# Kernel optimization log

Hardware: AMD Instinct MI355X
Metric: run time of the kernel (lower is better)

Reference implementation:

```python
import jax, jax.numpy as jnp
import numpy as np

N, E, F_IN, HID, HEADS, OUT, NGRAPH = 50000, 800000, 128, 64, 4, 64, 512
NEG_SLOPE = 0.2


def setup_inputs() -> dict:
    key = jax.random.key(0)
    ks = jax.random.split(key, 16)
    d1 = HID * HEADS  # 256
    inp = {
        "x": jax.random.normal(ks[0], (N, F_IN), jnp.float32),
        "edge_index": jax.random.randint(ks[1], (2, E), 0, N, jnp.int64),
        "batch": jnp.sort(jax.random.randint(ks[2], (N,), 0, NGRAPH, jnp.int64)),
        # layer 1 params (GATConv(F_IN -> HID, heads=HEADS, concat=True))
        "W1": jax.random.normal(ks[3], (F_IN, d1), jnp.float32) * 0.05,
        "att_src1": jax.random.normal(ks[4], (HEADS, HID), jnp.float32) * 0.05,
        "att_dst1": jax.random.normal(ks[5], (HEADS, HID), jnp.float32) * 0.05,
        "b1": jnp.zeros((d1,), jnp.float32),
        # layer 2 params (GATConv(d1 -> HID, heads=HEADS, concat=True))
        "W2": jax.random.normal(ks[6], (d1, d1), jnp.float32) * 0.05,
        "att_src2": jax.random.normal(ks[7], (HEADS, HID), jnp.float32) * 0.05,
        "att_dst2": jax.random.normal(ks[8], (HEADS, HID), jnp.float32) * 0.05,
        "b2": jnp.zeros((d1,), jnp.float32),
        # final linear
        "fc_w": jax.random.normal(ks[9], (d1, OUT), jnp.float32) * 0.05,
        "fc_b": jnp.zeros((OUT,), jnp.float32),
    }
    return inp


def _gat_layer(x, src, dst, W, att_src, att_dst, bias):
    # linear transform, split into heads: [N, H, C]
    h = (x @ W).reshape(N, HEADS, HID)
    # per-node attention logits (a^T h), per head: [N, H]
    a_s = jnp.einsum("nhc,hc->nh", h, att_src)
    a_d = jnp.einsum("nhc,hc->nh", h, att_dst)
    # per-edge logits with leaky relu: [E', H]
    e = a_s[src] + a_d[dst]
    e = jnp.where(e > 0, e, NEG_SLOPE * e)
    # segment softmax over edges grouped by destination node
    m = jax.ops.segment_max(e, dst, num_segments=N)
    ex = jnp.exp(e - m[dst])
    s = jax.ops.segment_sum(ex, dst, num_segments=N)
    alpha = ex / s[dst]  # every node has a self-loop -> s > 0
    # weighted message aggregation: scatter-add of alpha * h_src
    out = jax.ops.segment_sum(h[src] * alpha[:, :, None], dst, num_segments=N)
    return out.reshape(N, HEADS * HID) + bias


def reference(x, edge_index, batch, W1, att_src1, att_dst1, b1,
              W2, att_src2, att_dst2, b2, fc_w, fc_b):
    # PyG GATConv default add_self_loops=True
    loop = jnp.arange(N, dtype=edge_index.dtype)
    src = jnp.concatenate([edge_index[0], loop])
    dst = jnp.concatenate([edge_index[1], loop])

    h = _gat_layer(x, src, dst, W1, att_src1, att_dst1, b1)
    h = jax.nn.elu(h)  # dropout is identity in eval mode
    h = _gat_layer(h, src, dst, W2, att_src2, att_dst2, b2)
    h = jax.nn.elu(h)

    # global mean pool over graphs
    sums = jax.ops.segment_sum(h, batch, num_segments=NGRAPH)
    cnts = jax.ops.segment_sum(jnp.ones((N,), h.dtype), batch, num_segments=NGRAPH)
    pooled = sums / jnp.maximum(cnts, 1.0)[:, None]

    return pooled @ fc_w + fc_b
```

## Files before the change

### kernel.cpp

```cpp
#include <hip/hip_runtime.h>
#include <cstddef>
#include <cstdint>

#define NN 50000
#define EE 800000
#define ETOT (EE + NN)
#define FIN 128
#define D1 256
#define HID 64
#define HEADS 4
#define NG 512
#define FOUT 64
#define NEG_SLOPE 0.2f

typedef _Float16 f16x8 __attribute__((ext_vector_type(8)));
typedef _Float16 f16x4 __attribute__((ext_vector_type(4)));
typedef float f32x4 __attribute__((ext_vector_type(4)));

__device__ __forceinline__ float leaky(float x) { return x > 0.f ? x : NEG_SLOPE * x; }

__global__ void k_hist(const int* __restrict__ ei, int* __restrict__ deg) {
    int e = blockIdx.x * 256 + threadIdx.x;
    if (e < EE) atomicAdd(&deg[ei[EE + e]], 1);
}

__global__ void k_scan_blocks(const int* __restrict__ deg, int* __restrict__ row_off,
                              int* __restrict__ part) {
    __shared__ int sd[256];
    int tid = threadIdx.x;
    int i = blockIdx.x * 256 + tid;
    int v = (i < NN) ? deg[i] + 1 : 0;
    sd[tid] = v;
    __syncthreads();
    for (int off = 1; off < 256; off <<= 1) {
        int t = (tid >= off) ? sd[tid - off] : 0;
        __syncthreads();
        sd[tid] += t;
        __syncthreads();
    }
    if (i < NN) row_off[i] = sd[tid] - v;
    if (tid == 255) part[blockIdx.x] = sd[255];
}

__global__ void k_scan_part(int* __restrict__ part) {
    __shared__ int sd[256];
    int tid = threadIdx.x;
    int nblk = (NN + 255) / 256;
    int v = (tid < nblk) ? part[tid] : 0;
    sd[tid] = v;
    __syncthreads();
    for (int off = 1; off < 256; off <<= 1) {
        int t = (tid >= off) ? sd[tid - off] : 0;
        __syncthreads();
        sd[tid] += t;
        __syncthreads();
    }
    part[tid] = sd[tid] - v;
}

__global__ void k_add_off(int* __restrict__ row_off, const int* __restrict__ part,
                          int* __restrict__ cursor) {
    int i = blockIdx.x * 256 + threadIdx.x;
    if (i < NN) {
        int r = row_off[i] + part[blockIdx.x];
        row_off[i] = r;
        cursor[i] = r;
    }
    if (i == 0) row_off[NN] = ETOT;
}

__global__ void k_scatter(const int* __restrict__ ei, int* __restrict__ cursor,
                          int* __restrict__ csr_src) {
    int i = blockIdx.x * 256 + threadIdx.x;
    if (i < ETOT) {
        int s, d;
        if (i < EE) { s = ei[i]; d = ei[EE + i]; }
        else        { s = d = i - EE; }
        int p = atomicAdd(&cursor[d], 1);
        csr_src[p] = s;
    }
}

__global__ void k_cvt_w(const float* __restrict__ W1, const float* __restrict__ W2,
                        _Float16* __restrict__ w1t, _Float16* __restrict__ w2t) {
    int idx = blockIdx.x * 256 + threadIdx.x;
    if (idx < 256 * FIN) {
        int n = idx / FIN, k = idx - n * FIN;
        w1t[idx] = (_Float16)W1[(size_t)k * 256 + n];
    } else if (idx < 256 * FIN + 256 * D1) {
        int j = idx - 256 * FIN;
        int n = j >> 8, k = j & 255;
        w2t[j] = (_Float16)W2[(size_t)k * 256 + n];
    }
}

#define BM 128
#define BN 128
#define BK 64
#define LDK (BK + 4)

template <int K, typename AT>
__global__ __launch_bounds__(256) void k_gemm(const AT* __restrict__ A,
                                              const _Float16* __restrict__ Bt,
                                              _Float16* __restrict__ C,
                                              const float* __restrict__ att_s,
                                              const float* __restrict__ att_d,
                                              float* __restrict__ a_s,
                                              float* __restrict__ a_d) {
    __shared__ _Float16 As[BM][LDK];
    __shared__ _Float16 Bs[BN][LDK];
    const int tid = threadIdx.x;
    const int lane = tid & 63;
    const int wave = tid >> 6;
    const int wm = wave & 1, wn = wave >> 1;
    const int m0 = blockIdx.x * BM;
    const int n0 = blockIdx.y * BN;
    const int row_m = lane & 15, quad = lane >> 4;

    f32x4 acc[4][4];
#pragma unroll
    for (int mi = 0; mi < 4; ++mi)
#pragma unroll
        for (int ni = 0; ni < 4; ++ni)
#pragma unroll
            for (int r = 0; r < 4; ++r) acc[mi][ni][r] = 0.f;

    const int c8 = (tid & 7) * 8;
    const int rr = tid >> 3;

    for (int k0 = 0; k0 < K; k0 += BK) {
#pragma unroll
        for (int p = 0; p < 4; ++p) {
            int r = p * 32 + rr;
            int gr = m0 + r; gr = gr < NN ? gr : NN - 1;
            f16x8 o;
            if constexpr (sizeof(AT) == 4) {
                const float4 v0 = *(const float4*)((const float*)A + (size_t)gr * K + k0 + c8);
                const float4 v1 = *(const float4*)((const float*)A + (size_t)gr * K + k0 + c8 + 4);
                o[0] = (_Float16)v0.x; o[1] = (_Float16)v0.y;
                o[2] = (_Float16)v0.z; o[3] = (_Float16)v0.w;
                o[4] = (_Float16)v1.x; o[5] = (_Float16)v1.y;
                o[6] = (_Float16)v1.z; o[7] = (_Float16)v1.w;
            } else {
                o = *(const f16x8*)((const _Float16*)A + (size_t)gr * K + k0 + c8);
            }
            *(f16x8*)(&As[r][c8]) = o;
        }
#pragma unroll
        for (int p = 0; p < 4; ++p) {
            int r = p * 32 + rr;
            f16x8 v = *(const f16x8*)(Bt + (size_t)(n0 + r) * K + k0 + c8);
            *(f16x8*)(&Bs[r][c8]) = v;
        }
        __syncthreads();
#pragma unroll
        for (int kc = 0; kc < BK; kc += 32) {
            f16x8 af[4], bf[4];
#pragma unroll
            for (int mi = 0; mi < 4; ++mi)
                af[mi] = *(const f16x8*)(&As[wm * 64 + mi * 16 + row_m][kc + quad * 8]);
#pragma unroll
            for (int ni = 0; ni < 4; ++ni)
                bf[ni] = *(const f16x8*)(&Bs[wn * 64 + ni * 16 + row_m][kc + quad * 8]);
#pragma unroll
            for (int mi = 0; mi < 4; ++mi)
#pragma unroll
                for (int ni = 0; ni < 4; ++ni)
                    acc[mi][ni] = __builtin_amdgcn_mfma_f32_16x16x32_f16(
                        bf[ni], af[mi], acc[mi][ni], 0, 0, 0);
        }
        __syncthreads();
    }
#pragma unroll
    for (int mi = 0; mi < 4; ++mi) {
        int m = m0 + wm * 64 + mi * 16 + row_m;
        if (m < NN) {
#pragma unroll
            for (int ni = 0; ni < 4; ++ni) {
                f16x4 o;
                o[0] = (_Float16)acc[mi][ni][0];
                o[1] = (_Float16)acc[mi][ni][1];
                o[2] = (_Float16)acc[mi][ni][2];
                o[3] = (_Float16)acc[mi][ni][3];
                *(f16x4*)(C + (size_t)m * D1 + n0 + wn * 64 + ni * 16 + quad * 4) = o;
            }
        }
    }
    const int head = blockIdx.y * 2 + wn;
    const float* attsv = att_s + head * HID;
    const float* attdv = att_d + head * HID;
    float avs[4][4], avd[4][4];
#pragma unroll
    for (int ni = 0; ni < 4; ++ni)
#pragma unroll
        for (int r = 0; r < 4; ++r) {
            avs[ni][r] = attsv[ni * 16 + quad * 4 + r];
            avd[ni][r] = attdv[ni * 16 + quad * 4 + r];
        }
#pragma unroll
    for (int mi = 0; mi < 4; ++mi) {
        float ps = 0.f, pd = 0.f;
#pragma unroll
        for (int ni = 0; ni < 4; ++ni)
#pragma unroll
            for (int r = 0; r < 4; ++r) {
                ps += acc[mi][ni][r] * avs[ni][r];
                pd += acc[mi][ni][r] * avd[ni][r];
            }
        ps += __shfl_xor(ps, 16); ps += __shfl_xor(ps, 32);
        pd += __shfl_xor(pd, 16); pd += __shfl_xor(pd, 32);
        int m = m0 + wm * 64 + mi * 16 + row_m;
        if (quad == 0 && m < NN) {
            a_s[m * 4 + head] = ps;
            a_d[m * 4 + head] = pd;
        }
    }
}

__global__ __launch_bounds__(64) void k_aggregate(
    const _Float16* __restrict__ h, const float* __restrict__ a_s,
    const float* __restrict__ a_d, const int* __restrict__ row_off,
    const int* __restrict__ csr_src, const float* __restrict__ bias,
    _Float16* __restrict__ out, int apply_elu) {
    const int n = blockIdx.x;
    const int tid = threadIdx.x;
    const int myhead = tid >> 4;
    const int start = row_off[n];
    const int end = row_off[n + 1];

    __shared__ float s_w[64][4];
    __shared__ int s_src[64];

    const float4 ad = *(const float4*)(a_d + (size_t)n * 4);

    float l0 = 0.f, l1 = 0.f, l2 = 0.f, l3 = 0.f;
    float4 acc = make_float4(0.f, 0.f, 0.f, 0.f);
    const int c4 = tid * 4;
    for (int base = start; base < end; base += 64) {
        int len = min(64, end - base);
        if (tid < len) {
            int s = csr_src[base + tid];
            const float4 as = *(const float4*)(a_s + (size_t)s * 4);
            float x0 = __expf(leaky(as.x + ad.x));
            float x1 = __expf(leaky(as.y + ad.y));
            float x2 = __expf(leaky(as.z + ad.z));
            float x3 = __expf(leaky(as.w + ad.w));
            l0 += x0; l1 += x1; l2 += x2; l3 += x3;
            s_src[tid] = s;
            s_w[tid][0] = x0; s_w[tid][1] = x1; s_w[tid][2] = x2; s_w[tid][3] = x3;
        }
        __syncthreads();
#pragma unroll 4
        for (int jj = 0; jj < len; ++jj) {
            float wgt = s_w[jj][myhead];
            const f16x4 hv = *(const f16x4*)(h + (size_t)s_src[jj] * D1 + c4);
            acc.x += wgt * (float)hv[0];
            acc.y += wgt * (float)hv[1];
            acc.z += wgt * (float)hv[2];
            acc.w += wgt * (float)hv[3];
        }
        __syncthreads();
    }
#pragma unroll
    for (int off = 32; off > 0; off >>= 1) {
        l0 += __shfl_down(l0, off);
        l1 += __shfl_down(l1, off);
        l2 += __shfl_down(l2, off);
        l3 += __shfl_down(l3, off);
    }
    l0 = __shfl(l0, 0); l1 = __shfl(l1, 0); l2 = __shfl(l2, 0); l3 = __shfl(l3, 0);
    float denom = (myhead == 0) ? l0 : (myhead == 1) ? l1 : (myhead == 2) ? l2 : l3;
    float inv = 1.f / denom;

    const float4 bb = *(const float4*)(bias + c4);
    float vx = acc.x * inv + bb.x;
    float vy = acc.y * inv + bb.y;
    float vz = acc.z * inv + bb.z;
    float vw = acc.w * inv + bb.w;
    if (apply_elu) {
        vx = vx > 0.f ? vx : expm1f(vx);
        vy = vy > 0.f ? vy : expm1f(vy);
        vz = vz > 0.f ? vz : expm1f(vz);
        vw = vw > 0.f ? vw : expm1f(vw);
    }
    f16x4 o;
    o[0] = (_Float16)vx; o[1] = (_Float16)vy; o[2] = (_Float16)vz; o[3] = (_Float16)vw;
    *(f16x4*)(out + (size_t)n * D1 + c4) = o;
}

__global__ __launch_bounds__(256) void k_pool_fc(const _Float16* __restrict__ h,
                                                 const int* __restrict__ batch,
                                                 const float* __restrict__ fc_w,
                                                 const float* __restrict__ fc_b,
                                                 float* __restrict__ out) {
    __shared__ float row[D1];
    int g = blockIdx.x, c = threadIdx.x;
    int lo = 0, hi = NN;
    while (lo < hi) { int mid = (lo + hi) >> 1; if (batch[mid] < g) lo = mid + 1; else hi = mid; }
    int start = lo;
    hi = NN;
    while (lo < hi) { int mid = (lo + hi) >> 1; if (batch[mid] < g + 1) lo = mid + 1; else hi = mid; }
    int end = lo;

    float acc = 0.f;
    for (int n = start; n < end; ++n) acc += (float)h[(size_t)n * D1 + c];
    float inv = 1.f / fmaxf((float)(end - start), 1.f);
    row[c] = acc * inv;
    __syncthreads();
    if (c < FOUT) {
        float o = 0.f;
#pragma unroll 4
        for (int k = 0; k < D1; ++k) o += row[k] * fc_w[k * FOUT + c];
        out[(size_t)g * FOUT + c] = o + fc_b[c];
    }
}

extern "C" void kernel_launch(void* const* d_in, const int* in_sizes, int n_in,
                              void* d_out, int out_size, void* d_ws, size_t ws_size,
                              hipStream_t stream) {
    const float* x        = (const float*)d_in[0];
    const int*   ei       = (const int*)d_in[1];
    const int*   batch    = (const int*)d_in[2];
    const float* W1       = (const float*)d_in[3];
    const float* att_src1 = (const float*)d_in[4];
    const float* att_dst1 = (const float*)d_in[5];
    const float* b1       = (const float*)d_in[6];
    const float* W2       = (const float*)d_in[7];
    const float* att_src2 = (const float*)d_in[8];
    const float* att_dst2 = (const float*)d_in[9];
    const float* b2       = (const float*)d_in[10];
    const float* fc_w     = (const float*)d_in[11];
    const float* fc_b     = (const float*)d_in[12];
    float* out = (float*)d_out;

    _Float16* h_pre  = (_Float16*)d_ws;
    _Float16* h_act  = h_pre + (size_t)NN * D1;
    _Float16* w1t    = h_act + (size_t)NN * D1;
    _Float16* w2t    = w1t + 256 * FIN;
    float* a_s       = (float*)(w2t + 256 * D1);
    float* a_d       = a_s + (size_t)NN * 4;
    int*   deg       = (int*)(a_d + (size_t)NN * 4);
    int*   row_off   = deg + NN;
    int*   cursor    = row_off + NN + 1;
    int*   part      = cursor + NN;
    int*   csr_src   = part + 256;

    const int nblk_nodes = (NN + 255) / 256;
    const int nblk_edges = (EE + 255) / 256;
    const int nblk_etot  = (ETOT + 255) / 256;

    hipMemsetAsync(deg, 0, NN * sizeof(int), stream);
    k_hist<<<nblk_edges, 256, 0, stream>>>(ei, deg);
    k_scan_blocks<<<nblk_nodes, 256, 0, stream>>>(deg, row_off, part);
    k_scan_part<<<1, 256, 0, stream>>>(part);
    k_add_off<<<nblk_nodes, 256, 0, stream>>>(row_off, part, cursor);
    k_scatter<<<nblk_etot, 256, 0, stream>>>(ei, cursor, csr_src);

    k_cvt_w<<<(256 * (FIN + D1) + 255) / 256, 256, 0, stream>>>(W1, W2, w1t, w2t);

    dim3 ggrid((NN + BM - 1) / BM, D1 / BN);

    k_gemm<FIN, float><<<ggrid, 256, 0, stream>>>(x, w1t, h_pre,
                                                  att_src1, att_dst1, a_s, a_d);
    k_aggregate<<<NN, 64, 0, stream>>>(h_pre, a_s, a_d, row_off, csr_src, b1, h_act, 1);

    k_gemm<D1, _Float16><<<ggrid, 256, 0, stream>>>(h_act, w2t, h_pre,
                                                    att_src2, att_dst2, a_s, a_d);
    k_aggregate<<<NN, 64, 0, stream>>>(h_pre, a_s, a_d, row_off, csr_src, b2, h_act, 1);

    k_pool_fc<<<NG, 256, 0, stream>>>(h_act, batch, fc_w, fc_b, out);
}
```

Baseline: 407.1 us.

## Split aggregation per node into two channel-half blocks with dual-edge lanes

The aggregate kernel now launches two blocks per node, each covering two heads (128 channels). Within a block, the two 32-lane halves process alternate edges and combine their partial sums with a cross-lane shuffle. This halves the serial gather loop length per block and doubles the number of blocks, aiming to expose more memory parallelism. The cost is that each edge's source index and attention logits are read by both blocks, and there is extra shuffle and padding work.

```diff
diff --git a/kernel.cpp b/kernel.cpp
--- a/kernel.cpp
+++ b/kernel.cpp
@@ -222,38 +222,44 @@
     const float* __restrict__ a_d, const int* __restrict__ row_off,
     const int* __restrict__ csr_src, const float* __restrict__ bias,
     _Float16* __restrict__ out, int apply_elu) {
-    const int n = blockIdx.x;
+    const int b = blockIdx.x;
+    const int n = b >> 1;
+    const int half = b & 1;
     const int tid = threadIdx.x;
-    const int myhead = tid >> 4;
+    const int eoff = tid >> 5;
+    const int ln = tid & 31;
+    const int c4 = half * 128 + ln * 4;
+    const int hl = ln >> 4;
     const int start = row_off[n];
     const int end = row_off[n + 1];
 
-    __shared__ float s_w[64][4];
+    __shared__ float s_w[64][2];
     __shared__ int s_src[64];
 
-    const float4 ad = *(const float4*)(a_d + (size_t)n * 4);
-
-    float l0 = 0.f, l1 = 0.f, l2 = 0.f, l3 = 0.f;
+    const float2 ad = *(const float2*)(a_d + (size_t)n * 4 + half * 2);
+
+    float l0 = 0.f, l1 = 0.f;
     float4 acc = make_float4(0.f, 0.f, 0.f, 0.f);
-    const int c4 = tid * 4;
     for (int base = start; base < end; base += 64) {
         int len = min(64, end - base);
         if (tid < len) {
             int s = csr_src[base + tid];
-            const float4 as = *(const float4*)(a_s + (size_t)s * 4);
+            const float2 as = *(const float2*)(a_s + (size_t)s * 4 + half * 2);
             float x0 = __expf(leaky(as.x + ad.x));
             float x1 = __expf(leaky(as.y + ad.y));
-            float x2 = __expf(leaky(as.z + ad.z));
-            float x3 = __expf(leaky(as.w + ad.w));
-            l0 += x0; l1 += x1; l2 += x2; l3 += x3;
+            l0 += x0; l1 += x1;
             s_src[tid] = s;
-            s_w[tid][0] = x0; s_w[tid][1] = x1; s_w[tid][2] = x2; s_w[tid][3] = x3;
+            s_w[tid][0] = x0; s_w[tid][1] = x1;
+        } else {
+            s_src[tid] = 0;
+            s_w[tid][0] = 0.f; s_w[tid][1] = 0.f;
         }
         __syncthreads();
 #pragma unroll 4
-        for (int jj = 0; jj < len; ++jj) {
-            float wgt = s_w[jj][myhead];
-            const f16x4 hv = *(const f16x4*)(h + (size_t)s_src[jj] * D1 + c4);
+        for (int jj = 0; jj < len; jj += 2) {
+            const int je = jj + eoff;
+            const float wgt = s_w[je][hl];
+            const f16x4 hv = *(const f16x4*)(h + (size_t)s_src[je] * D1 + c4);
             acc.x += wgt * (float)hv[0];
             acc.y += wgt * (float)hv[1];
             acc.z += wgt * (float)hv[2];
@@ -261,31 +267,34 @@
         }
         __syncthreads();
     }
+    acc.x += __shfl_xor(acc.x, 32);
+    acc.y += __shfl_xor(acc.y, 32);
+    acc.z += __shfl_xor(acc.z, 32);
+    acc.w += __shfl_xor(acc.w, 32);
 #pragma unroll
     for (int off = 32; off > 0; off >>= 1) {
-        l0 += __shfl_down(l0, off);
-        l1 += __shfl_down(l1, off);
-        l2 += __shfl_down(l2, off);
-        l3 += __shfl_down(l3, off);
-    }
-    l0 = __shfl(l0, 0); l1 = __shfl(l1, 0); l2 = __shfl(l2, 0); l3 = __shfl(l3, 0);
-    float denom = (myhead == 0) ? l0 : (myhead == 1) ? l1 : (myhead == 2) ? l2 : l3;
-    float inv = 1.f / denom;
-
-    const float4 bb = *(const float4*)(bias + c4);
-    float vx = acc.x * inv + bb.x;
-    float vy = acc.y * inv + bb.y;
-    float vz = acc.z * inv + bb.z;
-    float vw = acc.w * inv + bb.w;
-    if (apply_elu) {
-        vx = vx > 0.f ? vx : expm1f(vx);
-        vy = vy > 0.f ? vy : expm1f(vy);
-        vz = vz > 0.f ? vz : expm1f(vz);
-        vw = vw > 0.f ? vw : expm1f(vw);
-    }
-    f16x4 o;
-    o[0] = (_Float16)vx; o[1] = (_Float16)vy; o[2] = (_Float16)vz; o[3] = (_Float16)vw;
-    *(f16x4*)(out + (size_t)n * D1 + c4) = o;
+        l0 += __shfl_xor(l0, off);
+        l1 += __shfl_xor(l1, off);
+    }
+
+    if (tid < 32) {
+        const float denom = (hl == 0) ? l0 : l1;
+        const float inv = 1.f / denom;
+        const float4 bb = *(const float4*)(bias + c4);
+        float vx = acc.x * inv + bb.x;
+        float vy = acc.y * inv + bb.y;
+        float vz = acc.z * inv + bb.z;
+        float vw = acc.w * inv + bb.w;
+        if (apply_elu) {
+            vx = vx > 0.f ? vx : expm1f(vx);
+            vy = vy > 0.f ? vy : expm1f(vy);
+            vz = vz > 0.f ? vz : expm1f(vz);
+            vw = vw > 0.f ? vw : expm1f(vw);
+        }
+        f16x4 o;
+        o[0] = (_Float16)vx; o[1] = (_Float16)vy; o[2] = (_Float16)vz; o[3] = (_Float16)vw;
+        *(f16x4*)(out + (size_t)n * D1 + c4) = o;
+    }
 }
 
 __global__ __launch_bounds__(256) void k_pool_fc(const _Float16* __restrict__ h,
@@ -362,11 +371,11 @@
 
     k_gemm<FIN, float><<<ggrid, 256, 0, stream>>>(x, w1t, h_pre,
                                                   att_src1, att_dst1, a_s, a_d);
-    k_aggregate<<<NN, 64, 0, stream>>>(h_pre, a_s, a_d, row_off, csr_src, b1, h_act, 1);
+    k_aggregate<<<2 * NN, 64, 0, stream>>>(h_pre, a_s, a_d, row_off, csr_src, b1, h_act, 1);
 
     k_gemm<D1, _Float16><<<ggrid, 256, 0, stream>>>(h_act, w2t, h_pre,
                                                     att_src2, att_dst2, a_s, a_d);
-    k_aggregate<<<NN, 64, 0, stream>>>(h_pre, a_s, a_d, row_off, csr_src, b2, h_act, 1);
+    k_aggregate<<<2 * NN, 64, 0, stream>>>(h_pre, a_s, a_d, row_off, csr_src, b2, h_act, 1);
 
     k_pool_fc<<<NG, 256, 0, stream>>>(h_act, batch, fc_w, fc_b, out);
 }
```

New measurement: 395.7 us. 2.8% less time.

## Precompute edge attention weights in separate kernel, drop shared-memory staging in aggregate

Applied to the files above, without the earlier changes.

Adds a kernel that computes the unnormalized exp attention weights per CSR edge and writes them to a workspace buffer. The aggregation kernel then loops directly over edges, reading the source index and weight from global memory, and no longer stages them in shared memory or uses block barriers and shuffle reductions. Each lane accumulates its own head's denominator. The trade is an extra kernel launch per layer and an extra write and read of about 850K×4 floats, against the removal of barriers and the serialized exp phase inside each aggregation block.

```diff
diff --git a/kernel.cpp b/kernel.cpp
--- a/kernel.cpp
+++ b/kernel.cpp
@@ -217,61 +217,52 @@
     }
 }
 
+__global__ __launch_bounds__(256) void k_edge_w(
+    const float* __restrict__ a_s, const float* __restrict__ a_d,
+    const int* __restrict__ row_off, const int* __restrict__ csr_src,
+    float* __restrict__ w_edge) {
+    const int n = blockIdx.x * 4 + (threadIdx.x >> 6);
+    const int lane = threadIdx.x & 63;
+    const int start = row_off[n];
+    const int end = row_off[n + 1];
+    const float4 ad = *(const float4*)(a_d + (size_t)n * 4);
+    for (int j = start + lane; j < end; j += 64) {
+        const int s = csr_src[j];
+        const float4 as = *(const float4*)(a_s + (size_t)s * 4);
+        float4 w;
+        w.x = __expf(leaky(as.x + ad.x));
+        w.y = __expf(leaky(as.y + ad.y));
+        w.z = __expf(leaky(as.z + ad.z));
+        w.w = __expf(leaky(as.w + ad.w));
+        *(float4*)(w_edge + (size_t)j * 4) = w;
+    }
+}
+
 __global__ __launch_bounds__(64) void k_aggregate(
-    const _Float16* __restrict__ h, const float* __restrict__ a_s,
-    const float* __restrict__ a_d, const int* __restrict__ row_off,
-    const int* __restrict__ csr_src, const float* __restrict__ bias,
-    _Float16* __restrict__ out, int apply_elu) {
+    const _Float16* __restrict__ h, const float* __restrict__ w_edge,
+    const int* __restrict__ row_off, const int* __restrict__ csr_src,
+    const float* __restrict__ bias, _Float16* __restrict__ out, int apply_elu) {
     const int n = blockIdx.x;
     const int tid = threadIdx.x;
     const int myhead = tid >> 4;
+    const int c4 = tid * 4;
     const int start = row_off[n];
     const int end = row_off[n + 1];
 
-    __shared__ float s_w[64][4];
-    __shared__ int s_src[64];
-
-    const float4 ad = *(const float4*)(a_d + (size_t)n * 4);
-
-    float l0 = 0.f, l1 = 0.f, l2 = 0.f, l3 = 0.f;
     float4 acc = make_float4(0.f, 0.f, 0.f, 0.f);
-    const int c4 = tid * 4;
-    for (int base = start; base < end; base += 64) {
-        int len = min(64, end - base);
-        if (tid < len) {
-            int s = csr_src[base + tid];
-            const float4 as = *(const float4*)(a_s + (size_t)s * 4);
-            float x0 = __expf(leaky(as.x + ad.x));
-            float x1 = __expf(leaky(as.y + ad.y));
-            float x2 = __expf(leaky(as.z + ad.z));
-            float x3 = __expf(leaky(as.w + ad.w));
-            l0 += x0; l1 += x1; l2 += x2; l3 += x3;
-            s_src[tid] = s;
-            s_w[tid][0] = x0; s_w[tid][1] = x1; s_w[tid][2] = x2; s_w[tid][3] = x3;
-        }
-        __syncthreads();
+    float l = 0.f;
 #pragma unroll 4
-        for (int jj = 0; jj < len; ++jj) {
-            float wgt = s_w[jj][myhead];
-            const f16x4 hv = *(const f16x4*)(h + (size_t)s_src[jj] * D1 + c4);
-            acc.x += wgt * (float)hv[0];
-            acc.y += wgt * (float)hv[1];
-            acc.z += wgt * (float)hv[2];
-            acc.w += wgt * (float)hv[3];
-        }
-        __syncthreads();
-    }
-#pragma unroll
-    for (int off = 32; off > 0; off >>= 1) {
-        l0 += __shfl_down(l0, off);
-        l1 += __shfl_down(l1, off);
-        l2 += __shfl_down(l2, off);
-        l3 += __shfl_down(l3, off);
-    }
-    l0 = __shfl(l0, 0); l1 = __shfl(l1, 0); l2 = __shfl(l2, 0); l3 = __shfl(l3, 0);
-    float denom = (myhead == 0) ? l0 : (myhead == 1) ? l1 : (myhead == 2) ? l2 : l3;
-    float inv = 1.f / denom;
-
+    for (int j = start; j < end; ++j) {
+        const int s = csr_src[j];
+        const float w = w_edge[(size_t)j * 4 + myhead];
+        const f16x4 hv = *(const f16x4*)(h + ((size_t)s << 8) + c4);
+        l += w;
+        acc.x += w * (float)hv[0];
+        acc.y += w * (float)hv[1];
+        acc.z += w * (float)hv[2];
+        acc.w += w * (float)hv[3];
+    }
+    const float inv = 1.f / l;
     const float4 bb = *(const float4*)(bias + c4);
     float vx = acc.x * inv + bb.x;
     float vy = acc.y * inv + bb.y;
@@ -344,6 +335,7 @@
     int*   cursor    = row_off + NN + 1;
     int*   part      = cursor + NN;
     int*   csr_src   = part + 256;
+    float* w_edge    = (float*)(csr_src + ETOT);
 
     const int nblk_nodes = (NN + 255) / 256;
     const int nblk_edges = (EE + 255) / 256;
@@ -362,11 +354,13 @@
 
     k_gemm<FIN, float><<<ggrid, 256, 0, stream>>>(x, w1t, h_pre,
                                                   att_src1, att_dst1, a_s, a_d);
-    k_aggregate<<<NN, 64, 0, stream>>>(h_pre, a_s, a_d, row_off, csr_src, b1, h_act, 1);
+    k_edge_w<<<NN / 4, 256, 0, stream>>>(a_s, a_d, row_off, csr_src, w_edge);
+    k_aggregate<<<NN, 64, 0, stream>>>(h_pre, w_edge, row_off, csr_src, b1, h_act, 1);
 
     k_gemm<D1, _Float16><<<ggrid, 256, 0, stream>>>(h_act, w2t, h_pre,
                                                     att_src2, att_dst2, a_s, a_d);
-    k_aggregate<<<NN, 64, 0, stream>>>(h_pre, a_s, a_d, row_off, csr_src, b2, h_act, 1);
+    k_edge_w<<<NN / 4, 256, 0, stream>>>(a_s, a_d, row_off, csr_src, w_edge);
+    k_aggregate<<<NN, 64, 0, stream>>>(h_pre, w_edge, row_off, csr_src, b2, h_act, 1);
 
     k_pool_fc<<<NG, 256, 0, stream>>>(h_act, batch, fc_w, fc_b, out);
 }
```

New measurement: 423.6 us. 1.04x slower.

## Two-pass bucketed CSR build and per-lane softmax denominator in aggregation

Applied to the files above, without the earlier changes.

Builds the CSR in two passes. Edges are first scattered into 16-node buckets, stored as (src,dst) pairs in a temp buffer, and then placed by per-node atomics. This is meant to make the final csr_src writes more local and cache friendly than fully random scatter. The aggregation kernel drops the shared source-index array and the cross-lane reduction of the softmax denominators. Each lane instead reads csr_src from global memory and accumulates its own head's weight sum inside the gather loop. The cost is an extra kernel, an extra temp buffer and an extra global index read per edge.

```diff
diff --git a/kernel.cpp b/kernel.cpp
--- a/kernel.cpp
+++ b/kernel.cpp
@@ -12,6 +12,7 @@
 #define NG 512
 #define FOUT 64
 #define NEG_SLOPE 0.2f
+#define NBUCK ((NN + 15) / 16)
 
 typedef _Float16 f16x8 __attribute__((ext_vector_type(8)));
 typedef _Float16 f16x4 __attribute__((ext_vector_type(4)));
@@ -59,25 +60,36 @@
 }
 
 __global__ void k_add_off(int* __restrict__ row_off, const int* __restrict__ part,
-                          int* __restrict__ cursor) {
+                          int* __restrict__ cursor, int* __restrict__ bcur) {
     int i = blockIdx.x * 256 + threadIdx.x;
     if (i < NN) {
         int r = row_off[i] + part[blockIdx.x];
         row_off[i] = r;
         cursor[i] = r;
+        if ((i & 15) == 0) bcur[i >> 4] = r;
     }
     if (i == 0) row_off[NN] = ETOT;
 }
 
-__global__ void k_scatter(const int* __restrict__ ei, int* __restrict__ cursor,
-                          int* __restrict__ csr_src) {
+__global__ void k_bucket(const int* __restrict__ ei, int* __restrict__ bcur,
+                         int2* __restrict__ tmp) {
     int i = blockIdx.x * 256 + threadIdx.x;
     if (i < ETOT) {
         int s, d;
         if (i < EE) { s = ei[i]; d = ei[EE + i]; }
         else        { s = d = i - EE; }
-        int p = atomicAdd(&cursor[d], 1);
-        csr_src[p] = s;
+        int p = atomicAdd(&bcur[d >> 4], 1);
+        tmp[p] = make_int2(s, d);
+    }
+}
+
+__global__ void k_place(const int2* __restrict__ tmp, int* __restrict__ cursor,
+                        int* __restrict__ csr_src) {
+    int i = blockIdx.x * 256 + threadIdx.x;
+    if (i < ETOT) {
+        int2 e = tmp[i];
+        int p = atomicAdd(&cursor[e.y], 1);
+        csr_src[p] = e.x;
     }
 }
 
@@ -225,53 +237,41 @@
     const int n = blockIdx.x;
     const int tid = threadIdx.x;
     const int myhead = tid >> 4;
+    const int c4 = tid * 4;
     const int start = row_off[n];
     const int end = row_off[n + 1];
 
     __shared__ float s_w[64][4];
-    __shared__ int s_src[64];
 
     const float4 ad = *(const float4*)(a_d + (size_t)n * 4);
 
-    float l0 = 0.f, l1 = 0.f, l2 = 0.f, l3 = 0.f;
     float4 acc = make_float4(0.f, 0.f, 0.f, 0.f);
-    const int c4 = tid * 4;
+    float l = 0.f;
     for (int base = start; base < end; base += 64) {
-        int len = min(64, end - base);
+        const int len = min(64, end - base);
         if (tid < len) {
-            int s = csr_src[base + tid];
+            const int s = csr_src[base + tid];
             const float4 as = *(const float4*)(a_s + (size_t)s * 4);
-            float x0 = __expf(leaky(as.x + ad.x));
-            float x1 = __expf(leaky(as.y + ad.y));
-            float x2 = __expf(leaky(as.z + ad.z));
-            float x3 = __expf(leaky(as.w + ad.w));
-            l0 += x0; l1 += x1; l2 += x2; l3 += x3;
-            s_src[tid] = s;
-            s_w[tid][0] = x0; s_w[tid][1] = x1; s_w[tid][2] = x2; s_w[tid][3] = x3;
+            s_w[tid][0] = __expf(leaky(as.x + ad.x));
+            s_w[tid][1] = __expf(leaky(as.y + ad.y));
+            s_w[tid][2] = __expf(leaky(as.z + ad.z));
+            s_w[tid][3] = __expf(leaky(as.w + ad.w));
         }
         __syncthreads();
 #pragma unroll 4
         for (int jj = 0; jj < len; ++jj) {
-            float wgt = s_w[jj][myhead];
-            const f16x4 hv = *(const f16x4*)(h + (size_t)s_src[jj] * D1 + c4);
-            acc.x += wgt * (float)hv[0];
-            acc.y += wgt * (float)hv[1];
-            acc.z += wgt * (float)hv[2];
-            acc.w += wgt * (float)hv[3];
-        }
-        __syncthreads();
-    }
-#pragma unroll
-    for (int off = 32; off > 0; off >>= 1) {
-        l0 += __shfl_down(l0, off);
-        l1 += __shfl_down(l1, off);
-        l2 += __shfl_down(l2, off);
-        l3 += __shfl_down(l3, off);
-    }
-    l0 = __shfl(l0, 0); l1 = __shfl(l1, 0); l2 = __shfl(l2, 0); l3 = __shfl(l3, 0);
-    float denom = (myhead == 0) ? l0 : (myhead == 1) ? l1 : (myhead == 2) ? l2 : l3;
-    float inv = 1.f / denom;
-
+            const int s = csr_src[base + jj];
+            const float w = s_w[jj][myhead];
+            const f16x4 hv = *(const f16x4*)(h + ((size_t)s << 8) + c4);
+            l += w;
+            acc.x += w * (float)hv[0];
+            acc.y += w * (float)hv[1];
+            acc.z += w * (float)hv[2];
+            acc.w += w * (float)hv[3];
+        }
+        __syncthreads();
+    }
+    const float inv = 1.f / l;
     const float4 bb = *(const float4*)(bias + c4);
     float vx = acc.x * inv + bb.x;
     float vy = acc.y * inv + bb.y;
@@ -343,7 +343,9 @@
     int*   row_off   = deg + NN;
     int*   cursor    = row_off + NN + 1;
     int*   part      = cursor + NN;
-    int*   csr_src   = part + 256;
+    int*   bcur      = part + 256;
+    int*   csr_src   = bcur + NBUCK;
+    int2*  tmp       = (int2*)(csr_src + ETOT);
 
     const int nblk_nodes = (NN + 255) / 256;
     const int nblk_edges = (EE + 255) / 256;
@@ -353,8 +355,9 @@
     k_hist<<<nblk_edges, 256, 0, stream>>>(ei, deg);
     k_scan_blocks<<<nblk_nodes, 256, 0, stream>>>(deg, row_off, part);
     k_scan_part<<<1, 256, 0, stream>>>(part);
-    k_add_off<<<nblk_nodes, 256, 0, stream>>>(row_off, part, cursor);
-    k_scatter<<<nblk_etot, 256, 0, stream>>>(ei, cursor, csr_src);
+    k_add_off<<<nblk_nodes, 256, 0, stream>>>(row_off, part, cursor, bcur);
+    k_bucket<<<nblk_etot, 256, 0, stream>>>(ei, bcur, tmp);
+    k_place<<<nblk_etot, 256, 0, stream>>>(tmp, cursor, csr_src);
 
     k_cvt_w<<<(256 * (FIN + D1) + 255) / 256, 256, 0, stream>>>(W1, W2, w1t, w2t);
 
```

After: 460.6 us. +13.1%, slower.
